# Kernel optimization log

Measured on AMD Instinct MI355X. Metric: run time of the kernel, lower is better.

## Reference

```python
import jax, jax.numpy as jnp
import numpy as np

D_MODEL = 256
D_FFN = 1024
N_HEADS = 8
N_LEVELS = 4
N_POINTS = 4
SPATIAL = np.array([[60, 100], [30, 50], [15, 25], [8, 13]], dtype=np.int32)  # (H, W) per level


def _layer_norm(x, g, b, eps=1e-5):
    mu = jnp.mean(x, axis=-1, keepdims=True)
    var = jnp.mean(jnp.square(x - mu), axis=-1, keepdims=True)
    return (x - mu) * jax.lax.rsqrt(var + eps) * g + b


def _bilinear_sample(v_l, loc, aw, H, W):
    # v_l: (B,H,W,h,hd); loc: (B,Lq,h,p,2) normalized [0,1]; aw: (B,Lq,h,p)
    B = v_l.shape[0]
    h = v_l.shape[3]
    x = loc[..., 0] * W - 0.5  # grid_sample align_corners=False convention
    y = loc[..., 1] * H - 0.5
    x0 = jnp.floor(x)
    y0 = jnp.floor(y)
    lx = x - x0
    ly = y - y0
    x0i = x0.astype(jnp.int32)
    y0i = y0.astype(jnp.int32)
    bi = jnp.arange(B)[:, None, None, None]
    hi = jnp.arange(h)[None, None, :, None]

    def g(xi, yi):
        valid = (xi >= 0) & (xi < W) & (yi >= 0) & (yi < H)
        xc = jnp.clip(xi, 0, W - 1)
        yc = jnp.clip(yi, 0, H - 1)
        return v_l[bi, yc, xc, hi] * valid[..., None].astype(v_l.dtype)  # zero padding

    w00 = (1 - lx) * (1 - ly)
    w01 = lx * (1 - ly)
    w10 = (1 - lx) * ly
    w11 = lx * ly
    samp = (g(x0i, y0i) * w00[..., None] + g(x0i + 1, y0i) * w01[..., None]
            + g(x0i, y0i + 1) * w10[..., None] + g(x0i + 1, y0i + 1) * w11[..., None])
    # weighted sum over sampling points -> (B,Lq,h,hd)
    return jnp.einsum('blhpd,blhp->blhd', samp, aw)


def _msda(q, val, ref, W_value, b_value, W_off, b_off, W_attn, b_attn, W_out, b_out):
    # mmcv MultiScaleDeformableAttention (batch_first, identity=query, eval-mode dropout)
    B, Lq, C = q.shape
    hd = C // N_HEADS
    v = (val @ W_value + b_value).reshape(B, -1, N_HEADS, hd)
    off = (q @ W_off + b_off).reshape(B, Lq, N_HEADS, N_LEVELS, N_POINTS, 2)
    aw = jax.nn.softmax((q @ W_attn + b_attn).reshape(B, Lq, N_HEADS, N_LEVELS * N_POINTS), axis=-1)
    aw = aw.reshape(B, Lq, N_HEADS, N_LEVELS, N_POINTS)
    normalizer = jnp.asarray(SPATIAL[:, ::-1].copy(), dtype=q.dtype)  # (levels, 2) = (W, H)
    loc = ref[:, :, None, :, None, :] + off / normalizer[None, None, None, :, None, :]
    out = jnp.zeros((B, Lq, N_HEADS, hd), q.dtype)
    start = 0
    for lvl in range(N_LEVELS):
        H, W = int(SPATIAL[lvl, 0]), int(SPATIAL[lvl, 1])
        v_l = v[:, start:start + H * W].reshape(B, H, W, N_HEADS, hd)
        start += H * W
        out = out + _bilinear_sample(v_l, loc[:, :, :, lvl], aw[:, :, :, lvl], H, W)
    return q + out.reshape(B, Lq, C) @ W_out + b_out  # identity + output_proj


def setup_inputs() -> dict:
    key = jax.random.key(0)
    ks = jax.random.split(key, 16)
    bs, cams, nq = 1, 6, 6400
    l = int(SPATIAL.prod(axis=1).sum())
    s = 0.02
    inp = {
        'query': jax.random.normal(ks[0], (bs, nq, D_MODEL), jnp.float32),
        'key': jax.random.normal(ks[1], (bs, cams, l, D_MODEL), jnp.float32),
        'value': jax.random.normal(ks[2], (bs, cams, l, D_MODEL), jnp.float32),
        'reference_points_cam': jax.random.uniform(ks[3], (cams, bs, nq, N_LEVELS, 2), jnp.float32),
        'spatial_shapes': jnp.asarray(SPATIAL),
        'level_start_index': jnp.asarray(np.concatenate([[0], np.cumsum(SPATIAL.prod(axis=1))[:-1]]).astype(np.int32)),
        'bev_mask': jax.random.randint(ks[4], (cams, bs, nq, 4), 0, 2).astype(jnp.int32),
        'W_value': jax.random.normal(ks[5], (D_MODEL, D_MODEL), jnp.float32) * s,
        'b_value': jnp.zeros((D_MODEL,), jnp.float32),
        'W_off': jax.random.normal(ks[6], (D_MODEL, N_HEADS * N_LEVELS * N_POINTS * 2), jnp.float32) * s,
        'b_off': jax.random.normal(ks[7], (N_HEADS * N_LEVELS * N_POINTS * 2,), jnp.float32) * s,
        'W_attn': jax.random.normal(ks[8], (D_MODEL, N_HEADS * N_LEVELS * N_POINTS), jnp.float32) * s,
        'b_attn': jnp.zeros((N_HEADS * N_LEVELS * N_POINTS,), jnp.float32),
        'W_out': jax.random.normal(ks[9], (D_MODEL, D_MODEL), jnp.float32) * s,
        'b_out': jnp.zeros((D_MODEL,), jnp.float32),
        'ln1_g': jnp.ones((D_MODEL,), jnp.float32),
        'ln1_b': jnp.zeros((D_MODEL,), jnp.float32),
        'W1': jax.random.normal(ks[10], (D_MODEL, D_FFN), jnp.float32) * s,
        'b1': jnp.zeros((D_FFN,), jnp.float32),
        'W2': jax.random.normal(ks[11], (D_FFN, D_MODEL), jnp.float32) * s,
        'b2': jnp.zeros((D_MODEL,), jnp.float32),
        'ln2_g': jnp.ones((D_MODEL,), jnp.float32),
        'ln2_b': jnp.zeros((D_MODEL,), jnp.float32),
    }
    return inp


def reference(query, key, value, reference_points_cam, spatial_shapes, level_start_index, bev_mask,
              W_value, b_value, W_off, b_off, W_attn, b_attn, W_out, b_out,
              ln1_g, ln1_b, W1, b1, W2, b2, ln2_g, ln2_b):
    bs, nq, C = query.shape
    cams = key.shape[1]
    l = key.shape[2]
    # per-camera query visibility taken from batch element 0 (as in original)
    cam_mask = (bev_mask[:, 0].sum(-1) > 0).astype(query.dtype)  # (cams, nq)
    # rebatch via masking: equivalent to gather-to-padded since attention is per-query
    q_rb = (query[:, None] * cam_mask[None, :, :, None]).reshape(bs * cams, nq, C)
    ref_rb = (jnp.transpose(reference_points_cam, (1, 0, 2, 3, 4))
              * cam_mask[None, :, :, None, None]).reshape(bs * cams, nq, N_LEVELS, 2)
    val = value.reshape(bs * cams, l, C)
    attn = _msda(q_rb, val, ref_rb, W_value, b_value, W_off, b_off, W_attn, b_attn, W_out, b_out)
    attn = attn.reshape(bs, cams, nq, C)
    # scatter-add back (only visible camera contributions)
    slots = jnp.einsum('bknc,kn->bnc', attn, cam_mask)
    # visibility count (full bev_mask, per batch element)
    count = (bev_mask.sum(-1) > 0).astype(query.dtype)  # (cams, bs, nq)
    count = jnp.maximum(count.transpose(1, 2, 0).sum(-1), 1.0)  # (bs, nq)
    slots = slots / count[..., None]
    x = _layer_norm(slots + query, ln1_g, ln1_b)
    ffn = jax.nn.relu(x @ W1 + b1) @ W2 + b2
    return _layer_norm(x + ffn, ln2_g, ln2_b)
```

## Files before the change

### kernel.cpp

```cpp
#include <hip/hip_runtime.h>
#include <math.h>

#define NQ      6400
#define NCAMS   6
#define LTOT    7979
#define DM      256
#define DFFN    1024

typedef __attribute__((ext_vector_type(8))) short bf16x8;
typedef __attribute__((ext_vector_type(4))) float f32x4;

__device__ inline unsigned short f32_to_bf16(float f) {
    unsigned u = __float_as_uint(f);
    unsigned r = u + 0x7FFF + ((u >> 16) & 1);
    return (unsigned short)(r >> 16);
}

__global__ __launch_bounds__(256) void wt_kernel(
    const float* __restrict__ Wv, const float* __restrict__ Woff,
    const float* __restrict__ Wattn, const float* __restrict__ Wout,
    const float* __restrict__ W1, const float* __restrict__ W2,
    unsigned short* __restrict__ wsT)
{
    int b = blockIdx.x;
    const float* src; int K, N, t0, dstoff;
    if (b < 64)       { src = Wv;    K = 256;  N = 256;  t0 = 0;   dstoff = 0; }
    else if (b < 128) { src = Woff;  K = 256;  N = 256;  t0 = 64;  dstoff = 65536; }
    else if (b < 160) { src = Wattn; K = 256;  N = 128;  t0 = 128; dstoff = 131072; }
    else if (b < 224) { src = Wout;  K = 256;  N = 256;  t0 = 160; dstoff = 163840; }
    else if (b < 480) { src = W1;    K = 256;  N = 1024; t0 = 224; dstoff = 229376; }
    else              { src = W2;    K = 1024; N = 256;  t0 = 480; dstoff = 491520; }
    int t = b - t0;
    int ntn = N >> 5;
    int kt = t / ntn, nt = t - kt * ntn;
    __shared__ float tile[32][33];
    int tx = threadIdx.x & 31, ty = threadIdx.x >> 5;
    #pragma unroll
    for (int i = 0; i < 4; ++i)
        tile[ty + i * 8][tx] = src[(size_t)(kt * 32 + ty + i * 8) * N + nt * 32 + tx];
    __syncthreads();
    #pragma unroll
    for (int i = 0; i < 4; ++i) {
        int nn = nt * 32 + ty + i * 8;
        wsT[dstoff + (size_t)nn * K + kt * 32 + tx] = f32_to_bf16(tile[tx][ty + i * 8]);
    }
}

__global__ __launch_bounds__(256) void gemm_v_kernel(
    const float* __restrict__ A, const unsigned short* __restrict__ BT,
    const float* __restrict__ bias, unsigned short* __restrict__ Cb, int M)
{
    const int K = 256;
    __shared__ __align__(16) unsigned short As[128][40];
    __shared__ __align__(16) unsigned short Bs[128][40];

    const int tid  = threadIdx.x;
    const int wave = tid >> 6, lane = tid & 63;
    const int wm = wave >> 1, wn = wave & 1;
    const int quad = lane >> 4, l16 = lane & 15;
    const int m0 = blockIdx.y * 128, n0 = blockIdx.x * 128;

    f32x4 acc[4][4] = {};

    for (int k0 = 0; k0 < K; k0 += 32) {
        #pragma unroll
        for (int i = 0; i < 2; ++i) {
            int idx = tid + 256 * i;
            int r = idx >> 2, kc = (idx & 3) * 8;
            int gr = m0 + r;
            float4 f0, f1;
            if (gr < M) {
                f0 = *(const float4*)(A + (size_t)gr * K + k0 + kc);
                f1 = *(const float4*)(A + (size_t)gr * K + k0 + kc + 4);
            } else { f0 = make_float4(0,0,0,0); f1 = f0; }
            uint4 o;
            o.x = f32_to_bf16(f0.x) | ((unsigned)f32_to_bf16(f0.y) << 16);
            o.y = f32_to_bf16(f0.z) | ((unsigned)f32_to_bf16(f0.w) << 16);
            o.z = f32_to_bf16(f1.x) | ((unsigned)f32_to_bf16(f1.y) << 16);
            o.w = f32_to_bf16(f1.z) | ((unsigned)f32_to_bf16(f1.w) << 16);
            *(uint4*)&As[r][kc] = o;
        }
        #pragma unroll
        for (int i = 0; i < 2; ++i) {
            int idx = tid + 256 * i;
            int r = idx >> 2, kc = (idx & 3) * 8;
            *(uint4*)&Bs[r][kc] = *(const uint4*)(BT + (size_t)(n0 + r) * K + k0 + kc);
        }
        __syncthreads();
        bf16x8 af[4], bfr[4];
        #pragma unroll
        for (int mi = 0; mi < 4; ++mi)
            af[mi] = *(const bf16x8*)&As[wm * 64 + mi * 16 + l16][quad * 8];
        #pragma unroll
        for (int ni = 0; ni < 4; ++ni)
            bfr[ni] = *(const bf16x8*)&Bs[wn * 64 + ni * 16 + l16][quad * 8];
        #pragma unroll
        for (int mi = 0; mi < 4; ++mi)
            #pragma unroll
            for (int ni = 0; ni < 4; ++ni)
                acc[mi][ni] = __builtin_amdgcn_mfma_f32_16x16x32_bf16(
                    af[mi], bfr[ni], acc[mi][ni], 0, 0, 0);
        __syncthreads();
    }

    #pragma unroll
    for (int mi = 0; mi < 4; ++mi) {
        #pragma unroll
        for (int r = 0; r < 4; ++r) {
            int gm = m0 + wm * 64 + mi * 16 + quad * 4 + r;
            if (gm >= M) continue;
            int cam = gm / LTOT;
            int pix = gm - cam * LTOT;
            #pragma unroll
            for (int ni = 0; ni < 4; ++ni) {
                int gn = n0 + wn * 64 + ni * 16 + l16;
                int head = gn >> 5, ch = gn & 31;
                float v = acc[mi][ni][r] + bias[gn];
                Cb[(((size_t)(cam * 8 + head)) * LTOT + pix) * 32 + ch] = f32_to_bf16(v);
            }
        }
    }
}

__global__ __launch_bounds__(256) void qproj_kernel(
    const float* __restrict__ A, const unsigned short* __restrict__ WqT,
    const float* __restrict__ b_off, const float* __restrict__ b_attn,
    float* __restrict__ qoff, float* __restrict__ qaw)
{
    const int K = 256;
    __shared__ __align__(16) unsigned short As[64][40];
    __shared__ __align__(16) unsigned short Bs[128][40];

    const int tid  = threadIdx.x;
    const int wave = tid >> 6, lane = tid & 63;
    const int wm = wave >> 1, wn = wave & 1;
    const int quad = lane >> 4, l16 = lane & 15;
    const int m0 = blockIdx.y * 64, n0 = blockIdx.x * 128;
    const int is_attn = (n0 == 256);

    f32x4 acc[2][4] = {};

    for (int k0 = 0; k0 < K; k0 += 32) {
        {
            int r = tid >> 2, kc = (tid & 3) * 8;
            float4 f0 = *(const float4*)(A + (size_t)(m0 + r) * K + k0 + kc);
            float4 f1 = *(const float4*)(A + (size_t)(m0 + r) * K + k0 + kc + 4);
            uint4 o;
            o.x = f32_to_bf16(f0.x) | ((unsigned)f32_to_bf16(f0.y) << 16);
            o.y = f32_to_bf16(f0.z) | ((unsigned)f32_to_bf16(f0.w) << 16);
            o.z = f32_to_bf16(f1.x) | ((unsigned)f32_to_bf16(f1.y) << 16);
            o.w = f32_to_bf16(f1.z) | ((unsigned)f32_to_bf16(f1.w) << 16);
            *(uint4*)&As[r][kc] = o;
        }
        #pragma unroll
        for (int i = 0; i < 2; ++i) {
            int idx = tid + 256 * i;
            int r = idx >> 2, kc = (idx & 3) * 8;
            *(uint4*)&Bs[r][kc] = *(const uint4*)(WqT + (size_t)(n0 + r) * K + k0 + kc);
        }
        __syncthreads();
        bf16x8 af[2], bfr[4];
        #pragma unroll
        for (int mi = 0; mi < 2; ++mi)
            af[mi] = *(const bf16x8*)&As[wm * 32 + mi * 16 + l16][quad * 8];
        #pragma unroll
        for (int ni = 0; ni < 4; ++ni)
            bfr[ni] = *(const bf16x8*)&Bs[wn * 64 + ni * 16 + l16][quad * 8];
        #pragma unroll
        for (int mi = 0; mi < 2; ++mi)
            #pragma unroll
            for (int ni = 0; ni < 4; ++ni)
                acc[mi][ni] = __builtin_amdgcn_mfma_f32_16x16x32_bf16(
                    af[mi], bfr[ni], acc[mi][ni], 0, 0, 0);
        __syncthreads();
    }

    if (is_attn) {
        #pragma unroll
        for (int mi = 0; mi < 2; ++mi) {
            #pragma unroll
            for (int r = 0; r < 4; ++r) {
                int gm = m0 + wm * 32 + mi * 16 + quad * 4 + r;
                #pragma unroll
                for (int ni = 0; ni < 4; ++ni) {
                    int gn = wn * 64 + ni * 16 + l16;
                    float v = acc[mi][ni][r] + b_attn[gn];
                    float mx = v;
                    #pragma unroll
                    for (int s = 1; s < 16; s <<= 1)
                        mx = fmaxf(mx, __shfl_xor(mx, s, 64));
                    float e = __expf(v - mx);
                    float sum = e;
                    #pragma unroll
                    for (int s = 1; s < 16; s <<= 1)
                        sum += __shfl_xor(sum, s, 64);
                    qaw[(size_t)gm * 128 + gn] = e / sum;
                }
            }
        }
    } else {
        #pragma unroll
        for (int mi = 0; mi < 2; ++mi) {
            #pragma unroll
            for (int r = 0; r < 4; ++r) {
                int gm = m0 + wm * 32 + mi * 16 + quad * 4 + r;
                #pragma unroll
                for (int ni = 0; ni < 4; ++ni) {
                    int gn = n0 + wn * 64 + ni * 16 + l16;
                    qoff[(size_t)gm * 256 + gn] = acc[mi][ni][r] + b_off[gn];
                }
            }
        }
    }
}

__global__ __launch_bounds__(256) void sample_kernel(
    const unsigned short* __restrict__ vb,
    const float* __restrict__ qoff,
    const float* __restrict__ aw,
    const float* __restrict__ refpts,
    const int*   __restrict__ bev_mask,
    unsigned short* __restrict__ outsum,
    float* __restrict__ visb)
{
    const int bid = blockIdx.x;
    const int h   = bid & 7;
    const int q0  = (bid >> 3) * 16;
    const int tid = threadIdx.x;
    const int sq  = tid >> 4;
    const int tup = tid & 15;
    const int lvl = tup >> 2;
    const int n_s = q0 + sq;
    const int tg  = (tid >> 2) & 3;
    const int cg  = tid & 3;

    __shared__ int2  s_tab[2][4][272];
    __shared__ float s_vis[NCAMS][16];
    __shared__ int   s_cnt[NCAMS];
    __shared__ int   s_nvis[16];

    if (tid < 96) {
        int cam = tid >> 4, q = tid & 15;
        const int* bm = bev_mask + ((size_t)cam * NQ + q0 + q) * 4;
        s_vis[cam][q] = ((bm[0] + bm[1] + bm[2] + bm[3]) > 0) ? 1.f : 0.f;
    }
    __syncthreads();
    if (tid < NCAMS) {
        float s = 0.f;
        #pragma unroll
        for (int q = 0; q < 16; ++q) s += s_vis[tid][q];
        s_cnt[tid] = (int)s;
    }
    if (tid >= 32 && tid < 48) {
        int q = tid - 32;
        float s = 0.f;
        #pragma unroll
        for (int cam = 0; cam < NCAMS; ++cam) s += s_vis[cam][q];
        s_nvis[q] = (int)s;
    }
    __syncthreads();

    const float my_aw = aw[(size_t)n_s * 128 + h * 16 + tup];
    const float offx  = qoff[(size_t)n_s * 256 + h * 32 + tup * 2];
    const float offy  = qoff[(size_t)n_s * 256 + h * 32 + tup * 2 + 1];
    const int Wl   = (lvl == 0) ? 100 : (lvl == 1) ? 50 : (lvl == 2) ? 25 : 13;
    const int Hl   = (lvl == 0) ? 60  : (lvl == 1) ? 30 : (lvl == 2) ? 15 : 8;
    const int base = (lvl == 0) ? 0   : (lvl == 1) ? 6000 : (lvl == 2) ? 7500 : 7875;
    const float dx = offx / (float)Wl;
    const float dy = offy / (float)Hl;
    const int tabi = sq * 17 + tup;

    int vcams[NCAMS], nvc = 0;
    #pragma unroll
    for (int k = 0; k < NCAMS; ++k)
        if (s_cnt[k] > 0) vcams[nvc++] = k;

    auto build_tab = [&](int k, int buf) {
        const size_t rbase = (((size_t)k * NQ + n_s) * 4 + lvl) * 2;
        float fx = (refpts[rbase + 0] + dx) * (float)Wl - 0.5f;
        float fy = (refpts[rbase + 1] + dy) * (float)Hl - 0.5f;
        float x0f = floorf(fx), y0f = floorf(fy);
        float lx = fx - x0f, ly = fy - y0f;
        int x0 = (int)x0f, y0 = (int)y0f;
        int x1 = x0 + 1, y1 = y0 + 1;
        float wb = my_aw * s_vis[k][sq];
        float w00 = (1.f - lx) * (1.f - ly) * wb;
        float w01 = lx * (1.f - ly) * wb;
        float w10 = (1.f - lx) * ly * wb;
        float w11 = lx * ly * wb;
        bool vx0 = (x0 >= 0) & (x0 < Wl), vx1 = (x1 >= 0) & (x1 < Wl);
        bool vy0 = (y0 >= 0) & (y0 < Hl), vy1 = (y1 >= 0) & (y1 < Hl);
        s_tab[buf][0][tabi] = make_int2((vx0 & vy0) ? (base + y0 * Wl + x0) * 64 : 0,
                                        __float_as_int((vx0 & vy0) ? w00 : 0.f));
        s_tab[buf][1][tabi] = make_int2((vx1 & vy0) ? (base + y0 * Wl + x1) * 64 : 0,
                                        __float_as_int((vx1 & vy0) ? w01 : 0.f));
        s_tab[buf][2][tabi] = make_int2((vx0 & vy1) ? (base + y1 * Wl + x0) * 64 : 0,
                                        __float_as_int((vx0 & vy1) ? w10 : 0.f));
        s_tab[buf][3][tabi] = make_int2((vx1 & vy1) ? (base + y1 * Wl + x1) * 64 : 0,
                                        __float_as_int((vx1 & vy1) ? w11 : 0.f));
    };

    float a0 = 0.f, a1 = 0.f, a2 = 0.f, a3 = 0.f;
    float a4 = 0.f, a5 = 0.f, a6 = 0.f, a7 = 0.f;

    if (nvc > 0) build_tab(vcams[0], 0);
    __syncthreads();

    int pb = 0;
    for (int i = 0; i < nvc; ++i) {
        int k = vcams[i];
        if (i + 1 < nvc) build_tab(vcams[i + 1], pb ^ 1);
        const char* vkh = (const char*)vb + (size_t)(k * 8 + h) * (LTOT * 64) + cg * 16;
        #pragma unroll
        for (int j = 0; j < 4; ++j) {
            int ti = sq * 17 + tg * 4 + j;
            #pragma unroll
            for (int corner = 0; corner < 4; ++corner) {
                int2 t = s_tab[pb][corner][ti];
                float w = __int_as_float(t.y);
                uint4 d = *(const uint4*)(vkh + t.x);
                a0 += w * __uint_as_float(d.x << 16);
                a1 += w * __uint_as_float(d.x & 0xFFFF0000u);
                a2 += w * __uint_as_float(d.y << 16);
                a3 += w * __uint_as_float(d.y & 0xFFFF0000u);
                a4 += w * __uint_as_float(d.z << 16);
                a5 += w * __uint_as_float(d.z & 0xFFFF0000u);
                a6 += w * __uint_as_float(d.w << 16);
                a7 += w * __uint_as_float(d.w & 0xFFFF0000u);
            }
        }
        __syncthreads();
        pb ^= 1;
    }

    a0 += __shfl_xor(a0, 4, 64); a0 += __shfl_xor(a0, 8, 64);
    a1 += __shfl_xor(a1, 4, 64); a1 += __shfl_xor(a1, 8, 64);
    a2 += __shfl_xor(a2, 4, 64); a2 += __shfl_xor(a2, 8, 64);
    a3 += __shfl_xor(a3, 4, 64); a3 += __shfl_xor(a3, 8, 64);
    a4 += __shfl_xor(a4, 4, 64); a4 += __shfl_xor(a4, 8, 64);
    a5 += __shfl_xor(a5, 4, 64); a5 += __shfl_xor(a5, 8, 64);
    a6 += __shfl_xor(a6, 4, 64); a6 += __shfl_xor(a6, 8, 64);
    a7 += __shfl_xor(a7, 4, 64); a7 += __shfl_xor(a7, 8, 64);

    if ((tid & 12) == 0) {
        int nv = s_nvis[sq];
        float sc = 1.f / (float)(nv > 0 ? nv : 1);
        uint4 o;
        o.x = f32_to_bf16(a0 * sc) | ((unsigned)f32_to_bf16(a1 * sc) << 16);
        o.y = f32_to_bf16(a2 * sc) | ((unsigned)f32_to_bf16(a3 * sc) << 16);
        o.z = f32_to_bf16(a4 * sc) | ((unsigned)f32_to_bf16(a5 * sc) << 16);
        o.w = f32_to_bf16(a6 * sc) | ((unsigned)f32_to_bf16(a7 * sc) << 16);
        *(uint4*)(outsum + (size_t)n_s * 256 + h * 32 + cg * 8) = o;
    }
    if (h == 0 && tid < 16) visb[q0 + tid] = (s_nvis[tid] > 0) ? 1.f : 0.f;
}

__global__ __launch_bounds__(256) void projln1_kernel(
    const unsigned short* __restrict__ A, const unsigned short* __restrict__ BT,
    const float* __restrict__ query, const float* __restrict__ visb,
    const float* __restrict__ b_out, const float* __restrict__ g,
    const float* __restrict__ b,
    float* __restrict__ xout, unsigned short* __restrict__ xbf)
{
    const int K = 256;
    __shared__ __align__(16) unsigned short As[32][40];
    __shared__ __align__(16) unsigned short Bs[256][40];
    __shared__ float sred[2][4][4][2];
    __shared__ float ssred[2][4][4][2];
    __shared__ float s_mu[32], s_rs[32];

    const int tid  = threadIdx.x;
    const int wave = tid >> 6, lane = tid & 63;
    const int wm = wave >> 1, wn = wave & 1;
    const int quad = lane >> 4, l16 = lane & 15;
    const int m0 = blockIdx.x * 32;

    f32x4 acc[8] = {};

    for (int k0 = 0; k0 < K; k0 += 32) {
        {
            int r = tid >> 3, kc = (tid & 7) * 4;
            *(uint2*)&As[r][kc] = *(const uint2*)(A + (size_t)(m0 + r) * K + k0 + kc);
        }
        {
            const unsigned short* src = BT + (size_t)tid * K + k0;
            uint4 d0 = *(const uint4*)(src);
            uint4 d1 = *(const uint4*)(src + 8);
            uint4 d2 = *(const uint4*)(src + 16);
            uint4 d3 = *(const uint4*)(src + 24);
            *(uint4*)&Bs[tid][0]  = d0;
            *(uint4*)&Bs[tid][8]  = d1;
            *(uint4*)&Bs[tid][16] = d2;
            *(uint4*)&Bs[tid][24] = d3;
        }
        __syncthreads();
        bf16x8 af = *(const bf16x8*)&As[wm * 16 + l16][quad * 8];
        #pragma unroll
        for (int ni = 0; ni < 8; ++ni) {
            bf16x8 bfr = *(const bf16x8*)&Bs[wn * 128 + ni * 16 + l16][quad * 8];
            acc[ni] = __builtin_amdgcn_mfma_f32_16x16x32_bf16(af, bfr, acc[ni], 0, 0, 0);
        }
        __syncthreads();
    }

    float vals[8][4];
    #pragma unroll
    for (int r = 0; r < 4; ++r) {
        int gm = m0 + wm * 16 + quad * 4 + r;
        float vs = visb[gm];
        float s = 0.f, ss = 0.f;
        #pragma unroll
        for (int ni = 0; ni < 8; ++ni) {
            int gn = wn * 128 + ni * 16 + l16;
            float v = acc[ni][r] + vs * b_out[gn]
                    + query[(size_t)gm * 256 + gn] * (1.f + vs);
            vals[ni][r] = v;
            s += v; ss += v * v;
        }
        #pragma unroll
        for (int m = 1; m < 16; m <<= 1) {
            s  += __shfl_xor(s,  m, 64);
            ss += __shfl_xor(ss, m, 64);
        }
        if (l16 == 0) {
            sred[wm][quad][r][wn]  = s;
            ssred[wm][quad][r][wn] = ss;
        }
    }
    __syncthreads();
    if (tid < 32) {
        int lwm = tid >> 4, lq = (tid >> 2) & 3, lr = tid & 3;
        float s  = sred[lwm][lq][lr][0]  + sred[lwm][lq][lr][1];
        float ss = ssred[lwm][lq][lr][0] + ssred[lwm][lq][lr][1];
        float mu = s * (1.f / 256.f);
        float var = ss * (1.f / 256.f) - mu * mu;
        s_mu[tid] = mu;
        s_rs[tid] = rsqrtf(var + 1e-5f);
    }
    __syncthreads();

    #pragma unroll
    for (int r = 0; r < 4; ++r) {
        int rowl = wm * 16 + quad * 4 + r;
        int gm = m0 + rowl;
        float mu = s_mu[rowl], rs = s_rs[rowl];
        #pragma unroll
        for (int ni = 0; ni < 8; ++ni) {
            int gn = wn * 128 + ni * 16 + l16;
            float res = (vals[ni][r] - mu) * rs * g[gn] + b[gn];
            xout[(size_t)gm * 256 + gn] = res;
            xbf[(size_t)gm * 256 + gn] = f32_to_bf16(res);
        }
    }
}

__global__ __launch_bounds__(256) void gemm64_kernel(
    const unsigned short* __restrict__ A, const unsigned short* __restrict__ BT,
    const float* __restrict__ bias, float* __restrict__ C,
    unsigned short* __restrict__ Cb,
    int M, int N, int K, int mode)
{
    __shared__ __align__(16) unsigned short As[64][40];
    __shared__ __align__(16) unsigned short Bs[128][40];

    const int tid  = threadIdx.x;
    const int wave = tid >> 6, lane = tid & 63;
    const int wm = wave >> 1, wn = wave & 1;
    const int quad = lane >> 4, l16 = lane & 15;
    const int m0 = blockIdx.y * 64, n0 = blockIdx.x * 128;
    const int nz = gridDim.z;
    const int klen = K / nz;
    const int kbase = blockIdx.z * klen;

    f32x4 acc[2][4] = {};

    for (int k0 = kbase; k0 < kbase + klen; k0 += 32) {
        {
            int r = tid >> 2, kc = (tid & 3) * 8;
            int gr = m0 + r;
            uint4 d = (gr < M) ? *(const uint4*)(A + (size_t)gr * K + k0 + kc)
                               : make_uint4(0u, 0u, 0u, 0u);
            *(uint4*)&As[r][kc] = d;
        }
        #pragma unroll
        for (int i = 0; i < 2; ++i) {
            int idx = tid + 256 * i;
            int r = idx >> 2, kc = (idx & 3) * 8;
            *(uint4*)&Bs[r][kc] = *(const uint4*)(BT + (size_t)(n0 + r) * K + k0 + kc);
        }
        __syncthreads();
        bf16x8 af[2], bfr[4];
        #pragma unroll
        for (int mi = 0; mi < 2; ++mi)
            af[mi] = *(const bf16x8*)&As[wm * 32 + mi * 16 + l16][quad * 8];
        #pragma unroll
        for (int ni = 0; ni < 4; ++ni)
            bfr[ni] = *(const bf16x8*)&Bs[wn * 64 + ni * 16 + l16][quad * 8];
        #pragma unroll
        for (int mi = 0; mi < 2; ++mi)
            #pragma unroll
            for (int ni = 0; ni < 4; ++ni)
                acc[mi][ni] = __builtin_amdgcn_mfma_f32_16x16x32_bf16(
                    af[mi], bfr[ni], acc[mi][ni], 0, 0, 0);
        __syncthreads();
    }

    const float* bz = (blockIdx.z == 0) ? bias : nullptr;
    float* Cz = C ? (C + (size_t)blockIdx.z * M * N) : nullptr;

    #pragma unroll
    for (int mi = 0; mi < 2; ++mi) {
        #pragma unroll
        for (int r = 0; r < 4; ++r) {
            int gm = m0 + wm * 32 + mi * 16 + quad * 4 + r;
            if (gm >= M) continue;
            #pragma unroll
            for (int ni = 0; ni < 4; ++ni) {
                int gn = n0 + wn * 64 + ni * 16 + l16;
                float v = acc[mi][ni][r] + (bz ? bz[gn] : 0.f);
                if (mode == 1) {
                    Cb[(size_t)gm * N + gn] = f32_to_bf16(fmaxf(v, 0.f));
                } else {
                    Cz[(size_t)gm * N + gn] = v;
                }
            }
        }
    }
}

__device__ inline float block_sum_256(float v, float* red)
{
    #pragma unroll
    for (int o = 32; o > 0; o >>= 1) v += __shfl_down(v, o, 64);
    int lane = threadIdx.x & 63, w = threadIdx.x >> 6;
    if (lane == 0) red[w] = v;
    __syncthreads();
    float t = red[0] + red[1] + red[2] + red[3];
    __syncthreads();
    return t;
}

__global__ __launch_bounds__(256) void ln2_kernel(
    const float* __restrict__ x, const float* __restrict__ f0,
    const float* __restrict__ f1,
    const float* __restrict__ g, const float* __restrict__ b,
    float* __restrict__ out)
{
    __shared__ float red[4];
    int n = blockIdx.x, j = threadIdx.x;
    size_t idx = (size_t)n * 256 + j;
    float t = x[idx] + f0[idx] + f1[idx];
    float mu = block_sum_256(t, red) * (1.f / 256.f);
    float d = t - mu;
    float var = block_sum_256(d * d, red) * (1.f / 256.f);
    out[idx] = d * rsqrtf(var + 1e-5f) * g[j] + b[j];
}

extern "C" void kernel_launch(void* const* d_in, const int* in_sizes, int n_in,
                              void* d_out, int out_size, void* d_ws, size_t ws_size,
                              hipStream_t stream)
{
    const float* query   = (const float*)d_in[0];
    const float* value   = (const float*)d_in[2];
    const float* refpts  = (const float*)d_in[3];
    const int*   bevmask = (const int*)d_in[6];
    const float* W_value = (const float*)d_in[7];
    const float* b_value = (const float*)d_in[8];
    const float* W_off   = (const float*)d_in[9];
    const float* b_off   = (const float*)d_in[10];
    const float* W_attn  = (const float*)d_in[11];
    const float* b_attn  = (const float*)d_in[12];
    const float* W_out   = (const float*)d_in[13];
    const float* b_out   = (const float*)d_in[14];
    const float* ln1_g   = (const float*)d_in[15];
    const float* ln1_b   = (const float*)d_in[16];
    const float* W1      = (const float*)d_in[17];
    const float* b1      = (const float*)d_in[18];
    const float* W2      = (const float*)d_in[19];
    const float* b2      = (const float*)d_in[20];
    const float* ln2_g   = (const float*)d_in[21];
    const float* ln2_b   = (const float*)d_in[22];
    float* out = (float*)d_out;

    char* ws = (char*)d_ws;
    unsigned short* vb     = (unsigned short*)(ws + 0);
    float*          xbuf   = (float*)(ws + 0);
    unsigned short* xbf    = (unsigned short*)(ws + 7000000);
    unsigned short* hbf    = (unsigned short*)(ws + 11000000);
    float*          qoff   = (float*)(ws + 25000000);
    float*          qaw    = (float*)(ws + 32000000);
    unsigned short* outsum = (unsigned short*)(ws + 35300000);
    float*          visb   = (float*)(ws + 38600000);
    unsigned short* wsT    = (unsigned short*)(ws + 38700000);
    float*          ffnout = (float*)(ws + 41000000);

    unsigned short* WvT = wsT;
    unsigned short* WqT = wsT + 65536;
    unsigned short* WoT = wsT + 163840;
    unsigned short* W1T = wsT + 229376;
    unsigned short* W2T = wsT + 491520;

    const int MV = NCAMS * LTOT;

    wt_kernel<<<dim3(736), 256, 0, stream>>>(
        W_value, W_off, W_attn, W_out, W1, W2, wsT);
    gemm_v_kernel<<<dim3(2, (MV + 127) / 128), 256, 0, stream>>>(
        value, WvT, b_value, vb, MV);
    qproj_kernel<<<dim3(3, 100), 256, 0, stream>>>(
        query, WqT, b_off, b_attn, qoff, qaw);
    sample_kernel<<<dim3(3200), 256, 0, stream>>>(
        vb, qoff, qaw, refpts, bevmask, outsum, visb);
    projln1_kernel<<<dim3(200), 256, 0, stream>>>(
        outsum, WoT, query, visb, b_out, ln1_g, ln1_b, xbuf, xbf);
    gemm64_kernel<<<dim3(8, 100, 1), 256, 0, stream>>>(
        xbf, W1T, b1, nullptr, hbf, NQ, DFFN, 256, 1);
    gemm64_kernel<<<dim3(2, 100, 2), 256, 0, stream>>>(
        hbf, W2T, b2, ffnout, nullptr, NQ, 256, DFFN, 0);
    ln2_kernel<<<dim3(NQ), 256, 0, stream>>>(
        xbuf, ffnout, ffnout + (size_t)NQ * 256, ln2_g, ln2_b, out);
}
```

Measured before the change: 321.7 us.

## Fuse weight transpose, value and query projections into one launch; vectorize LN2

Merges the weight-transpose, value-projection GEMM and query-projection GEMM into a single heterogeneous head kernel. The value and query GEMMs now convert fp32 weights to bf16 directly while staging into shared memory, so the separate transpose pass is no longer needed for those weights. The sampling kernel builds lookup tables for all cameras up front instead of double-buffering them per camera, which trades a larger shared-memory footprint for fewer barriers. LayerNorm 2 is rewritten to use one wave per row with float4 loads and a single-pass sum/sum-of-squares variance, which is less numerically robust than the two-pass form.

```diff
diff --git a/kernel.cpp b/kernel.cpp
--- a/kernel.cpp
+++ b/kernel.cpp
@@ -16,200 +16,203 @@
     return (unsigned short)(r >> 16);
 }
 
-__global__ __launch_bounds__(256) void wt_kernel(
-    const float* __restrict__ Wv, const float* __restrict__ Woff,
-    const float* __restrict__ Wattn, const float* __restrict__ Wout,
-    const float* __restrict__ W1, const float* __restrict__ W2,
-    unsigned short* __restrict__ wsT)
+__global__ __launch_bounds__(256) void head_kernel(
+    const float* __restrict__ value, const float* __restrict__ query,
+    const float* __restrict__ Wv, const float* __restrict__ bv,
+    const float* __restrict__ Woff, const float* __restrict__ boff,
+    const float* __restrict__ Wattn, const float* __restrict__ battn,
+    const float* __restrict__ Wout, const float* __restrict__ W1,
+    const float* __restrict__ W2,
+    unsigned short* __restrict__ vb, float* __restrict__ qoff,
+    float* __restrict__ qaw, unsigned short* __restrict__ wsT)
 {
-    int b = blockIdx.x;
-    const float* src; int K, N, t0, dstoff;
-    if (b < 64)       { src = Wv;    K = 256;  N = 256;  t0 = 0;   dstoff = 0; }
-    else if (b < 128) { src = Woff;  K = 256;  N = 256;  t0 = 64;  dstoff = 65536; }
-    else if (b < 160) { src = Wattn; K = 256;  N = 128;  t0 = 128; dstoff = 131072; }
-    else if (b < 224) { src = Wout;  K = 256;  N = 256;  t0 = 160; dstoff = 163840; }
-    else if (b < 480) { src = W1;    K = 256;  N = 1024; t0 = 224; dstoff = 229376; }
-    else              { src = W2;    K = 1024; N = 256;  t0 = 480; dstoff = 491520; }
-    int t = b - t0;
-    int ntn = N >> 5;
-    int kt = t / ntn, nt = t - kt * ntn;
-    __shared__ float tile[32][33];
-    int tx = threadIdx.x & 31, ty = threadIdx.x >> 5;
-    #pragma unroll
-    for (int i = 0; i < 4; ++i)
-        tile[ty + i * 8][tx] = src[(size_t)(kt * 32 + ty + i * 8) * N + nt * 32 + tx];
-    __syncthreads();
-    #pragma unroll
-    for (int i = 0; i < 4; ++i) {
-        int nn = nt * 32 + ty + i * 8;
-        wsT[dstoff + (size_t)nn * K + kt * 32 + tx] = f32_to_bf16(tile[tx][ty + i * 8]);
-    }
-}
-
-__global__ __launch_bounds__(256) void gemm_v_kernel(
-    const float* __restrict__ A, const unsigned short* __restrict__ BT,
-    const float* __restrict__ bias, unsigned short* __restrict__ Cb, int M)
-{
-    const int K = 256;
-    __shared__ __align__(16) unsigned short As[128][40];
-    __shared__ __align__(16) unsigned short Bs[128][40];
-
-    const int tid  = threadIdx.x;
-    const int wave = tid >> 6, lane = tid & 63;
-    const int wm = wave >> 1, wn = wave & 1;
-    const int quad = lane >> 4, l16 = lane & 15;
-    const int m0 = blockIdx.y * 128, n0 = blockIdx.x * 128;
-
-    f32x4 acc[4][4] = {};
-
-    for (int k0 = 0; k0 < K; k0 += 32) {
-        #pragma unroll
-        for (int i = 0; i < 2; ++i) {
-            int idx = tid + 256 * i;
-            int r = idx >> 2, kc = (idx & 3) * 8;
-            int gr = m0 + r;
-            float4 f0, f1;
-            if (gr < M) {
-                f0 = *(const float4*)(A + (size_t)gr * K + k0 + kc);
-                f1 = *(const float4*)(A + (size_t)gr * K + k0 + kc + 4);
-            } else { f0 = make_float4(0,0,0,0); f1 = f0; }
-            uint4 o;
-            o.x = f32_to_bf16(f0.x) | ((unsigned)f32_to_bf16(f0.y) << 16);
-            o.y = f32_to_bf16(f0.z) | ((unsigned)f32_to_bf16(f0.w) << 16);
-            o.z = f32_to_bf16(f1.x) | ((unsigned)f32_to_bf16(f1.y) << 16);
-            o.w = f32_to_bf16(f1.z) | ((unsigned)f32_to_bf16(f1.w) << 16);
-            *(uint4*)&As[r][kc] = o;
-        }
-        #pragma unroll
-        for (int i = 0; i < 2; ++i) {
-            int idx = tid + 256 * i;
-            int r = idx >> 2, kc = (idx & 3) * 8;
-            *(uint4*)&Bs[r][kc] = *(const uint4*)(BT + (size_t)(n0 + r) * K + k0 + kc);
-        }
-        __syncthreads();
-        bf16x8 af[4], bfr[4];
-        #pragma unroll
-        for (int mi = 0; mi < 4; ++mi)
-            af[mi] = *(const bf16x8*)&As[wm * 64 + mi * 16 + l16][quad * 8];
-        #pragma unroll
-        for (int ni = 0; ni < 4; ++ni)
-            bfr[ni] = *(const bf16x8*)&Bs[wn * 64 + ni * 16 + l16][quad * 8];
-        #pragma unroll
-        for (int mi = 0; mi < 4; ++mi)
+    __shared__ __align__(16) unsigned char smem[20480];
+    const int b = blockIdx.x;
+    const int tid = threadIdx.x;
+
+    if (b < 750) {
+        unsigned short (*As)[40] = (unsigned short(*)[40])smem;
+        unsigned short (*Bs)[40] = (unsigned short(*)[40])(smem + 10240);
+        const int wave = tid >> 6, lane = tid & 63;
+        const int wm = wave >> 1, wn = wave & 1;
+        const int quad = lane >> 4, l16 = lane & 15;
+        const int m0 = (b >> 1) * 128, n0 = (b & 1) * 128;
+        const int M = NCAMS * LTOT;
+
+        f32x4 acc[4][4] = {};
+
+        for (int k0 = 0; k0 < 256; k0 += 32) {
+            #pragma unroll
+            for (int i = 0; i < 2; ++i) {
+                int idx = tid + 256 * i;
+                int r = idx >> 2, kc = (idx & 3) * 8;
+                int gr = m0 + r;
+                float4 f0, f1;
+                if (gr < M) {
+                    f0 = *(const float4*)(value + (size_t)gr * 256 + k0 + kc);
+                    f1 = *(const float4*)(value + (size_t)gr * 256 + k0 + kc + 4);
+                } else { f0 = make_float4(0.f,0.f,0.f,0.f); f1 = f0; }
+                uint4 o;
+                o.x = f32_to_bf16(f0.x) | ((unsigned)f32_to_bf16(f0.y) << 16);
+                o.y = f32_to_bf16(f0.z) | ((unsigned)f32_to_bf16(f0.w) << 16);
+                o.z = f32_to_bf16(f1.x) | ((unsigned)f32_to_bf16(f1.y) << 16);
+                o.w = f32_to_bf16(f1.z) | ((unsigned)f32_to_bf16(f1.w) << 16);
+                *(uint4*)&As[r][kc] = o;
+            }
+            #pragma unroll
+            for (int i = 0; i < 4; ++i) {
+                int idx = tid + 256 * i;
+                int kr = idx >> 5, c = (idx & 31) * 4;
+                float4 f = *(const float4*)(Wv + (size_t)(k0 + kr) * 256 + n0 + c);
+                Bs[c    ][kr] = f32_to_bf16(f.x);
+                Bs[c + 1][kr] = f32_to_bf16(f.y);
+                Bs[c + 2][kr] = f32_to_bf16(f.z);
+                Bs[c + 3][kr] = f32_to_bf16(f.w);
+            }
+            __syncthreads();
+            bf16x8 af[4], bfr[4];
+            #pragma unroll
+            for (int mi = 0; mi < 4; ++mi)
+                af[mi] = *(const bf16x8*)&As[wm * 64 + mi * 16 + l16][quad * 8];
             #pragma unroll
             for (int ni = 0; ni < 4; ++ni)
-                acc[mi][ni] = __builtin_amdgcn_mfma_f32_16x16x32_bf16(
-                    af[mi], bfr[ni], acc[mi][ni], 0, 0, 0);
-        __syncthreads();
-    }
-
-    #pragma unroll
-    for (int mi = 0; mi < 4; ++mi) {
-        #pragma unroll
-        for (int r = 0; r < 4; ++r) {
-            int gm = m0 + wm * 64 + mi * 16 + quad * 4 + r;
-            if (gm >= M) continue;
-            int cam = gm / LTOT;
-            int pix = gm - cam * LTOT;
-            #pragma unroll
-            for (int ni = 0; ni < 4; ++ni) {
-                int gn = n0 + wn * 64 + ni * 16 + l16;
-                int head = gn >> 5, ch = gn & 31;
-                float v = acc[mi][ni][r] + bias[gn];
-                Cb[(((size_t)(cam * 8 + head)) * LTOT + pix) * 32 + ch] = f32_to_bf16(v);
-            }
-        }
-    }
-}
-
-__global__ __launch_bounds__(256) void qproj_kernel(
-    const float* __restrict__ A, const unsigned short* __restrict__ WqT,
-    const float* __restrict__ b_off, const float* __restrict__ b_attn,
-    float* __restrict__ qoff, float* __restrict__ qaw)
-{
-    const int K = 256;
-    __shared__ __align__(16) unsigned short As[64][40];
-    __shared__ __align__(16) unsigned short Bs[128][40];
-
-    const int tid  = threadIdx.x;
-    const int wave = tid >> 6, lane = tid & 63;
-    const int wm = wave >> 1, wn = wave & 1;
-    const int quad = lane >> 4, l16 = lane & 15;
-    const int m0 = blockIdx.y * 64, n0 = blockIdx.x * 128;
-    const int is_attn = (n0 == 256);
-
-    f32x4 acc[2][4] = {};
-
-    for (int k0 = 0; k0 < K; k0 += 32) {
-        {
-            int r = tid >> 2, kc = (tid & 3) * 8;
-            float4 f0 = *(const float4*)(A + (size_t)(m0 + r) * K + k0 + kc);
-            float4 f1 = *(const float4*)(A + (size_t)(m0 + r) * K + k0 + kc + 4);
-            uint4 o;
-            o.x = f32_to_bf16(f0.x) | ((unsigned)f32_to_bf16(f0.y) << 16);
-            o.y = f32_to_bf16(f0.z) | ((unsigned)f32_to_bf16(f0.w) << 16);
-            o.z = f32_to_bf16(f1.x) | ((unsigned)f32_to_bf16(f1.y) << 16);
-            o.w = f32_to_bf16(f1.z) | ((unsigned)f32_to_bf16(f1.w) << 16);
-            *(uint4*)&As[r][kc] = o;
-        }
-        #pragma unroll
-        for (int i = 0; i < 2; ++i) {
-            int idx = tid + 256 * i;
-            int r = idx >> 2, kc = (idx & 3) * 8;
-            *(uint4*)&Bs[r][kc] = *(const uint4*)(WqT + (size_t)(n0 + r) * K + k0 + kc);
-        }
-        __syncthreads();
-        bf16x8 af[2], bfr[4];
-        #pragma unroll
-        for (int mi = 0; mi < 2; ++mi)
-            af[mi] = *(const bf16x8*)&As[wm * 32 + mi * 16 + l16][quad * 8];
-        #pragma unroll
-        for (int ni = 0; ni < 4; ++ni)
-            bfr[ni] = *(const bf16x8*)&Bs[wn * 64 + ni * 16 + l16][quad * 8];
-        #pragma unroll
-        for (int mi = 0; mi < 2; ++mi)
-            #pragma unroll
-            for (int ni = 0; ni < 4; ++ni)
-                acc[mi][ni] = __builtin_amdgcn_mfma_f32_16x16x32_bf16(
-                    af[mi], bfr[ni], acc[mi][ni], 0, 0, 0);
-        __syncthreads();
-    }
-
-    if (is_attn) {
-        #pragma unroll
-        for (int mi = 0; mi < 2; ++mi) {
+                bfr[ni] = *(const bf16x8*)&Bs[wn * 64 + ni * 16 + l16][quad * 8];
+            #pragma unroll
+            for (int mi = 0; mi < 4; ++mi)
+                #pragma unroll
+                for (int ni = 0; ni < 4; ++ni)
+                    acc[mi][ni] = __builtin_amdgcn_mfma_f32_16x16x32_bf16(
+                        af[mi], bfr[ni], acc[mi][ni], 0, 0, 0);
+            __syncthreads();
+        }
+
+        #pragma unroll
+        for (int mi = 0; mi < 4; ++mi) {
             #pragma unroll
             for (int r = 0; r < 4; ++r) {
-                int gm = m0 + wm * 32 + mi * 16 + quad * 4 + r;
-                #pragma unroll
-                for (int ni = 0; ni < 4; ++ni) {
-                    int gn = wn * 64 + ni * 16 + l16;
-                    float v = acc[mi][ni][r] + b_attn[gn];
-                    float mx = v;
-                    #pragma unroll
-                    for (int s = 1; s < 16; s <<= 1)
-                        mx = fmaxf(mx, __shfl_xor(mx, s, 64));
-                    float e = __expf(v - mx);
-                    float sum = e;
-                    #pragma unroll
-                    for (int s = 1; s < 16; s <<= 1)
-                        sum += __shfl_xor(sum, s, 64);
-                    qaw[(size_t)gm * 128 + gn] = e / sum;
-                }
-            }
-        }
-    } else {
-        #pragma unroll
-        for (int mi = 0; mi < 2; ++mi) {
-            #pragma unroll
-            for (int r = 0; r < 4; ++r) {
-                int gm = m0 + wm * 32 + mi * 16 + quad * 4 + r;
+                int gm = m0 + wm * 64 + mi * 16 + quad * 4 + r;
+                if (gm >= M) continue;
+                int cam = gm / LTOT;
+                int pix = gm - cam * LTOT;
                 #pragma unroll
                 for (int ni = 0; ni < 4; ++ni) {
                     int gn = n0 + wn * 64 + ni * 16 + l16;
-                    qoff[(size_t)gm * 256 + gn] = acc[mi][ni][r] + b_off[gn];
+                    int head = gn >> 5, ch = gn & 31;
+                    float v = acc[mi][ni][r] + bv[gn];
+                    vb[(((size_t)(cam * 8 + head)) * LTOT + pix) * 32 + ch] = f32_to_bf16(v);
                 }
             }
+        }
+    } else if (b < 1050) {
+        unsigned short (*As)[40] = (unsigned short(*)[40])smem;
+        unsigned short (*Bs)[40] = (unsigned short(*)[40])(smem + 5120);
+        const int t = b - 750;
+        const int bx = t / 100, by = t % 100;
+        const int wave = tid >> 6, lane = tid & 63;
+        const int wm = wave >> 1, wn = wave & 1;
+        const int quad = lane >> 4, l16 = lane & 15;
+        const int m0 = by * 64;
+        const int is_attn = (bx == 2);
+        const float* Wsrc  = is_attn ? Wattn : Woff;
+        const int   stride = is_attn ? 128 : 256;
+        const int   nbase  = is_attn ? 0 : bx * 128;
+
+        f32x4 acc[2][4] = {};
+
+        for (int k0 = 0; k0 < 256; k0 += 32) {
+            {
+                int r = tid >> 2, kc = (tid & 3) * 8;
+                float4 f0 = *(const float4*)(query + (size_t)(m0 + r) * 256 + k0 + kc);
+                float4 f1 = *(const float4*)(query + (size_t)(m0 + r) * 256 + k0 + kc + 4);
+                uint4 o;
+                o.x = f32_to_bf16(f0.x) | ((unsigned)f32_to_bf16(f0.y) << 16);
+                o.y = f32_to_bf16(f0.z) | ((unsigned)f32_to_bf16(f0.w) << 16);
+                o.z = f32_to_bf16(f1.x) | ((unsigned)f32_to_bf16(f1.y) << 16);
+                o.w = f32_to_bf16(f1.z) | ((unsigned)f32_to_bf16(f1.w) << 16);
+                *(uint4*)&As[r][kc] = o;
+            }
+            #pragma unroll
+            for (int i = 0; i < 4; ++i) {
+                int idx = tid + 256 * i;
+                int kr = idx >> 5, c = (idx & 31) * 4;
+                float4 f = *(const float4*)(Wsrc + (size_t)(k0 + kr) * stride + nbase + c);
+                Bs[c    ][kr] = f32_to_bf16(f.x);
+                Bs[c + 1][kr] = f32_to_bf16(f.y);
+                Bs[c + 2][kr] = f32_to_bf16(f.z);
+                Bs[c + 3][kr] = f32_to_bf16(f.w);
+            }
+            __syncthreads();
+            bf16x8 af[2], bfr[4];
+            #pragma unroll
+            for (int mi = 0; mi < 2; ++mi)
+                af[mi] = *(const bf16x8*)&As[wm * 32 + mi * 16 + l16][quad * 8];
+            #pragma unroll
+            for (int ni = 0; ni < 4; ++ni)
+                bfr[ni] = *(const bf16x8*)&Bs[wn * 64 + ni * 16 + l16][quad * 8];
+            #pragma unroll
+            for (int mi = 0; mi < 2; ++mi)
+                #pragma unroll
+                for (int ni = 0; ni < 4; ++ni)
+                    acc[mi][ni] = __builtin_amdgcn_mfma_f32_16x16x32_bf16(
+                        af[mi], bfr[ni], acc[mi][ni], 0, 0, 0);
+            __syncthreads();
+        }
+
+        if (is_attn) {
+            #pragma unroll
+            for (int mi = 0; mi < 2; ++mi) {
+                #pragma unroll
+                for (int r = 0; r < 4; ++r) {
+                    int gm = m0 + wm * 32 + mi * 16 + quad * 4 + r;
+                    #pragma unroll
+                    for (int ni = 0; ni < 4; ++ni) {
+                        int gn = wn * 64 + ni * 16 + l16;
+                        float v = acc[mi][ni][r] + battn[gn];
+                        float mx = v;
+                        #pragma unroll
+                        for (int s = 1; s < 16; s <<= 1)
+                            mx = fmaxf(mx, __shfl_xor(mx, s, 64));
+                        float e = __expf(v - mx);
+                        float sum = e;
+                        #pragma unroll
+                        for (int s = 1; s < 16; s <<= 1)
+                            sum += __shfl_xor(sum, s, 64);
+                        qaw[(size_t)gm * 128 + gn] = e / sum;
+                    }
+                }
+            }
+        } else {
+            #pragma unroll
+            for (int mi = 0; mi < 2; ++mi) {
+                #pragma unroll
+                for (int r = 0; r < 4; ++r) {
+                    int gm = m0 + wm * 32 + mi * 16 + quad * 4 + r;
+                    #pragma unroll
+                    for (int ni = 0; ni < 4; ++ni) {
+                        int gn = nbase + wn * 64 + ni * 16 + l16;
+                        qoff[(size_t)gm * 256 + gn] = acc[mi][ni][r] + boff[gn];
+                    }
+                }
+            }
+        }
+    } else {
+        float (*tile)[33] = (float(*)[33])smem;
+        int t = b - 1050;
+        const float* src; int K, N, dstoff;
+        if (t < 64)       { src = Wout; K = 256;  N = 256;  dstoff = 0; }
+        else if (t < 320) { src = W1;   K = 256;  N = 1024; dstoff = 65536;  t -= 64; }
+        else              { src = W2;   K = 1024; N = 256;  dstoff = 327680; t -= 320; }
+        int ntn = N >> 5;
+        int kt = t / ntn, nt = t - kt * ntn;
+        int tx = tid & 31, ty = tid >> 5;
+        #pragma unroll
+        for (int i = 0; i < 4; ++i)
+            tile[ty + i * 8][tx] = src[(size_t)(kt * 32 + ty + i * 8) * N + nt * 32 + tx];
+        __syncthreads();
+        #pragma unroll
+        for (int i = 0; i < 4; ++i) {
+            int nn = nt * 32 + ty + i * 8;
+            wsT[dstoff + (size_t)nn * K + kt * 32 + tx] = f32_to_bf16(tile[tx][ty + i * 8]);
         }
     }
 }
@@ -234,7 +237,7 @@
     const int tg  = (tid >> 2) & 3;
     const int cg  = tid & 3;
 
-    __shared__ int2  s_tab[2][4][272];
+    __shared__ int2  s_tab[NCAMS][4][272];
     __shared__ float s_vis[NCAMS][16];
     __shared__ int   s_cnt[NCAMS];
     __shared__ int   s_nvis[16];
@@ -258,7 +261,6 @@
         for (int cam = 0; cam < NCAMS; ++cam) s += s_vis[cam][q];
         s_nvis[q] = (int)s;
     }
-    __syncthreads();
 
     const float my_aw = aw[(size_t)n_s * 128 + h * 16 + tup];
     const float offx  = qoff[(size_t)n_s * 256 + h * 32 + tup * 2];
@@ -270,15 +272,16 @@
     const float dy = offy / (float)Hl;
     const int tabi = sq * 17 + tup;
 
-    int vcams[NCAMS], nvc = 0;
+    float2 rp[NCAMS];
     #pragma unroll
     for (int k = 0; k < NCAMS; ++k)
-        if (s_cnt[k] > 0) vcams[nvc++] = k;
-
-    auto build_tab = [&](int k, int buf) {
-        const size_t rbase = (((size_t)k * NQ + n_s) * 4 + lvl) * 2;
-        float fx = (refpts[rbase + 0] + dx) * (float)Wl - 0.5f;
-        float fy = (refpts[rbase + 1] + dy) * (float)Hl - 0.5f;
+        rp[k] = *(const float2*)(refpts + (((size_t)k * NQ + n_s) * 4 + lvl) * 2);
+    __syncthreads();
+
+    #pragma unroll
+    for (int k = 0; k < NCAMS; ++k) {
+        float fx = (rp[k].x + dx) * (float)Wl - 0.5f;
+        float fy = (rp[k].y + dy) * (float)Hl - 0.5f;
         float x0f = floorf(fx), y0f = floorf(fy);
         float lx = fx - x0f, ly = fy - y0f;
         int x0 = (int)x0f, y0 = (int)y0f;
@@ -290,33 +293,29 @@
         float w11 = lx * ly * wb;
         bool vx0 = (x0 >= 0) & (x0 < Wl), vx1 = (x1 >= 0) & (x1 < Wl);
         bool vy0 = (y0 >= 0) & (y0 < Hl), vy1 = (y1 >= 0) & (y1 < Hl);
-        s_tab[buf][0][tabi] = make_int2((vx0 & vy0) ? (base + y0 * Wl + x0) * 64 : 0,
-                                        __float_as_int((vx0 & vy0) ? w00 : 0.f));
-        s_tab[buf][1][tabi] = make_int2((vx1 & vy0) ? (base + y0 * Wl + x1) * 64 : 0,
-                                        __float_as_int((vx1 & vy0) ? w01 : 0.f));
-        s_tab[buf][2][tabi] = make_int2((vx0 & vy1) ? (base + y1 * Wl + x0) * 64 : 0,
-                                        __float_as_int((vx0 & vy1) ? w10 : 0.f));
-        s_tab[buf][3][tabi] = make_int2((vx1 & vy1) ? (base + y1 * Wl + x1) * 64 : 0,
-                                        __float_as_int((vx1 & vy1) ? w11 : 0.f));
-    };
+        s_tab[k][0][tabi] = make_int2((vx0 & vy0) ? (base + y0 * Wl + x0) * 64 : 0,
+                                      __float_as_int((vx0 & vy0) ? w00 : 0.f));
+        s_tab[k][1][tabi] = make_int2((vx1 & vy0) ? (base + y0 * Wl + x1) * 64 : 0,
+                                      __float_as_int((vx1 & vy0) ? w01 : 0.f));
+        s_tab[k][2][tabi] = make_int2((vx0 & vy1) ? (base + y1 * Wl + x0) * 64 : 0,
+                                      __float_as_int((vx0 & vy1) ? w10 : 0.f));
+        s_tab[k][3][tabi] = make_int2((vx1 & vy1) ? (base + y1 * Wl + x1) * 64 : 0,
+                                      __float_as_int((vx1 & vy1) ? w11 : 0.f));
+    }
+    __syncthreads();
 
     float a0 = 0.f, a1 = 0.f, a2 = 0.f, a3 = 0.f;
     float a4 = 0.f, a5 = 0.f, a6 = 0.f, a7 = 0.f;
 
-    if (nvc > 0) build_tab(vcams[0], 0);
-    __syncthreads();
-
-    int pb = 0;
-    for (int i = 0; i < nvc; ++i) {
-        int k = vcams[i];
-        if (i + 1 < nvc) build_tab(vcams[i + 1], pb ^ 1);
+    for (int k = 0; k < NCAMS; ++k) {
+        if (s_cnt[k] == 0) continue;
         const char* vkh = (const char*)vb + (size_t)(k * 8 + h) * (LTOT * 64) + cg * 16;
         #pragma unroll
         for (int j = 0; j < 4; ++j) {
             int ti = sq * 17 + tg * 4 + j;
             #pragma unroll
             for (int corner = 0; corner < 4; ++corner) {
-                int2 t = s_tab[pb][corner][ti];
+                int2 t = s_tab[k][corner][ti];
                 float w = __int_as_float(t.y);
                 uint4 d = *(const uint4*)(vkh + t.x);
                 a0 += w * __uint_as_float(d.x << 16);
@@ -329,8 +328,6 @@
                 a7 += w * __uint_as_float(d.w & 0xFFFF0000u);
             }
         }
-        __syncthreads();
-        pb ^= 1;
     }
 
     a0 += __shfl_xor(a0, 4, 64); a0 += __shfl_xor(a0, 8, 64);
@@ -384,14 +381,10 @@
         }
         {
             const unsigned short* src = BT + (size_t)tid * K + k0;
-            uint4 d0 = *(const uint4*)(src);
-            uint4 d1 = *(const uint4*)(src + 8);
-            uint4 d2 = *(const uint4*)(src + 16);
-            uint4 d3 = *(const uint4*)(src + 24);
-            *(uint4*)&Bs[tid][0]  = d0;
-            *(uint4*)&Bs[tid][8]  = d1;
-            *(uint4*)&Bs[tid][16] = d2;
-            *(uint4*)&Bs[tid][24] = d3;
+            *(uint4*)&Bs[tid][0]  = *(const uint4*)(src);
+            *(uint4*)&Bs[tid][8]  = *(const uint4*)(src + 8);
+            *(uint4*)&Bs[tid][16] = *(const uint4*)(src + 16);
+            *(uint4*)&Bs[tid][24] = *(const uint4*)(src + 24);
         }
         __syncthreads();
         bf16x8 af = *(const bf16x8*)&As[wm * 16 + l16][quad * 8];
@@ -528,32 +521,39 @@
     }
 }
 
-__device__ inline float block_sum_256(float v, float* red)
-{
-    #pragma unroll
-    for (int o = 32; o > 0; o >>= 1) v += __shfl_down(v, o, 64);
-    int lane = threadIdx.x & 63, w = threadIdx.x >> 6;
-    if (lane == 0) red[w] = v;
-    __syncthreads();
-    float t = red[0] + red[1] + red[2] + red[3];
-    __syncthreads();
-    return t;
-}
-
-__global__ __launch_bounds__(256) void ln2_kernel(
+__global__ __launch_bounds__(256) void ln2v_kernel(
     const float* __restrict__ x, const float* __restrict__ f0,
     const float* __restrict__ f1,
     const float* __restrict__ g, const float* __restrict__ b,
     float* __restrict__ out)
 {
-    __shared__ float red[4];
-    int n = blockIdx.x, j = threadIdx.x;
-    size_t idx = (size_t)n * 256 + j;
-    float t = x[idx] + f0[idx] + f1[idx];
-    float mu = block_sum_256(t, red) * (1.f / 256.f);
-    float d = t - mu;
-    float var = block_sum_256(d * d, red) * (1.f / 256.f);
-    out[idx] = d * rsqrtf(var + 1e-5f) * g[j] + b[j];
+    int row  = blockIdx.x * 4 + (threadIdx.x >> 6);
+    int lane = threadIdx.x & 63;
+    size_t base = (size_t)row * 256 + lane * 4;
+    float4 xv = *(const float4*)(x + base);
+    float4 av = *(const float4*)(f0 + base);
+    float4 cv = *(const float4*)(f1 + base);
+    float t0 = xv.x + av.x + cv.x;
+    float t1 = xv.y + av.y + cv.y;
+    float t2 = xv.z + av.z + cv.z;
+    float t3 = xv.w + av.w + cv.w;
+    float s  = t0 + t1 + t2 + t3;
+    float ss = t0 * t0 + t1 * t1 + t2 * t2 + t3 * t3;
+    #pragma unroll
+    for (int m = 1; m < 64; m <<= 1) {
+        s  += __shfl_xor(s,  m, 64);
+        ss += __shfl_xor(ss, m, 64);
+    }
+    float mu = s * (1.f / 256.f);
+    float rs = rsqrtf(ss * (1.f / 256.f) - mu * mu + 1e-5f);
+    float4 gv = *(const float4*)(g + lane * 4);
+    float4 bv = *(const float4*)(b + lane * 4);
+    float4 o;
+    o.x = (t0 - mu) * rs * gv.x + bv.x;
+    o.y = (t1 - mu) * rs * gv.y + bv.y;
+    o.z = (t2 - mu) * rs * gv.z + bv.z;
+    o.w = (t3 - mu) * rs * gv.w + bv.w;
+    *(float4*)(out + base) = o;
 }
 
 extern "C" void kernel_launch(void* const* d_in, const int* in_sizes, int n_in,
@@ -594,20 +594,13 @@
     unsigned short* wsT    = (unsigned short*)(ws + 38700000);
     float*          ffnout = (float*)(ws + 41000000);
 
-    unsigned short* WvT = wsT;
-    unsigned short* WqT = wsT + 65536;
-    unsigned short* WoT = wsT + 163840;
-    unsigned short* W1T = wsT + 229376;
-    unsigned short* W2T = wsT + 491520;
-
-    const int MV = NCAMS * LTOT;
-
-    wt_kernel<<<dim3(736), 256, 0, stream>>>(
-        W_value, W_off, W_attn, W_out, W1, W2, wsT);
-    gemm_v_kernel<<<dim3(2, (MV + 127) / 128), 256, 0, stream>>>(
-        value, WvT, b_value, vb, MV);
-    qproj_kernel<<<dim3(3, 100), 256, 0, stream>>>(
-        query, WqT, b_off, b_attn, qoff, qaw);
+    unsigned short* WoT = wsT;
+    unsigned short* W1T = wsT + 65536;
+    unsigned short* W2T = wsT + 327680;
+
+    head_kernel<<<dim3(1626), 256, 0, stream>>>(
+        value, query, W_value, b_value, W_off, b_off, W_attn, b_attn,
+        W_out, W1, W2, vb, qoff, qaw, wsT);
     sample_kernel<<<dim3(3200), 256, 0, stream>>>(
         vb, qoff, qaw, refpts, bevmask, outsum, visb);
     projln1_kernel<<<dim3(200), 256, 0, stream>>>(
@@ -616,6 +609,6 @@
         xbf, W1T, b1, nullptr, hbf, NQ, DFFN, 256, 1);
     gemm64_kernel<<<dim3(2, 100, 2), 256, 0, stream>>>(
         hbf, W2T, b2, ffnout, nullptr, NQ, 256, DFFN, 0);
-    ln2_kernel<<<dim3(NQ), 256, 0, stream>>>(
+    ln2v_kernel<<<dim3(1600), 256, 0, stream>>>(
         xbuf, ffnout, ffnout + (size_t)NQ * 256, ln2_g, ln2_b, out);
 }
```

Result: no change. 326.6 us (+1.5%).
